# Optimization experiments

Hardware: AMD Instinct MI355X
Metric: run time of the kernel (lower is better)

Reference implementation:

```python
import jax, jax.numpy as jnp
import numpy as np

NUM_LAYERS, NUM_HEADS, DH, C = 5, 4, 32, 128
B, T, HH, WW = 2, 12, 32, 32


def conv2d(x, w, b):
    # x: (N, Cin, H, W), w: (Cout, Cin, 3, 3) same padding
    y = jax.lax.conv_general_dilated(x, w, window_strides=(1, 1), padding='SAME',
                                     dimension_numbers=('NCHW', 'OIHW', 'NCHW'))
    return y + b[None, :, None, None]


def sine_pos(length, depth):
    pos = jnp.arange(length, dtype=jnp.float32)[:, None]
    div = jnp.exp(jnp.arange(0, depth, 2, dtype=jnp.float32) * (-np.log(10000.0) / depth))
    pe = jnp.zeros((length, depth), dtype=jnp.float32)
    pe = pe.at[:, 0::2].set(jnp.sin(pos * div))
    pe = pe.at[:, 1::2].set(jnp.cos(pos * div))
    return pe[None, :, :, None, None]  # (1, L, dh, 1, 1) broadcasts over batch & spatial


def group_norm(x, scale, bias, groups=4, eps=1e-5):
    n, c, h, w = x.shape
    xg = x.reshape(n, groups, c // groups, h, w)
    mu = xg.mean(axis=(2, 3, 4), keepdims=True)
    var = ((xg - mu) ** 2).mean(axis=(2, 3, 4), keepdims=True)
    xg = (xg - mu) * jax.lax.rsqrt(var + eps)
    return xg.reshape(n, c, h, w) * scale[None, :, None, None] + bias[None, :, None, None]


def head_forward(x, pos, qw, qb, kvw, kvb, aw, ab):
    # x: (B, L, dh, H, W)
    b, l, c, h, w = x.shape
    xf = x.reshape(b * l, c, h, w)
    q = conv2d(xf, qw, qb).reshape(b, l, c, h, w) + pos
    v = conv2d(xf, kvw, kvb).reshape(b, l, c, h, w)  # k and v share features
    k = v + pos
    # pairwise concat: (B, Lq, Lk, 2*dh, H, W)
    qe = jnp.broadcast_to(q[:, :, None], (b, l, l, c, h, w))
    ke = jnp.broadcast_to(k[:, None, :], (b, l, l, c, h, w))
    qk = jnp.concatenate([qe, ke], axis=3).reshape(b * l * l, 2 * c, h, w)
    att = conv2d(qk, aw, ab).reshape(b, l, l, 1, h, w)
    att = jax.nn.softmax(att, axis=2)  # softmax over key-frame axis
    return jnp.sum(att * v[:, None], axis=2)  # (B, L, dh, H, W)


def reference(input_tensor, q_w, q_b, kv_w, kv_b, att_w, att_b,
              ff1_w, ff1_b, ff2_w, ff2_b, gn_w, gn_b):
    num_layers, num_heads = q_w.shape[0], q_w.shape[1]
    b, l, c, h, w = input_tensor.shape
    dh = c // num_heads
    pos = sine_pos(l, dh)
    out = input_tensor
    for li in range(num_layers):
        heads = [head_forward(out[:, :, i * dh:(i + 1) * dh], pos,
                              q_w[li, i], q_b[li, i], kv_w[li, i], kv_b[li, i],
                              att_w[li, i], att_b[li, i])
                 for i in range(num_heads)]
        att_out = jnp.concatenate(heads, axis=2) + out  # residual
        att_flat = att_out.reshape(b * l, c, h, w)
        ff = conv2d(jax.nn.relu(conv2d(att_flat, ff1_w[li], ff1_b[li])), ff2_w[li], ff2_b[li])
        y = group_norm(ff + att_flat, gn_w[li], gn_b[li])
        out = y.reshape(b, l, c, h, w)
    return out


def setup_inputs() -> dict:
    key = jax.random.key(0)
    ks = jax.random.split(key, 12)
    f = lambda k, s, sc=1.0: jax.random.normal(k, s, dtype=jnp.float32) * sc
    L, H = NUM_LAYERS, NUM_HEADS
    return {
        'input_tensor': f(ks[0], (B, T, C, HH, WW)),
        'q_w': f(ks[1], (L, H, DH, DH, 3, 3), 0.05),
        'q_b': f(ks[2], (L, H, DH), 0.05),
        'kv_w': f(ks[3], (L, H, DH, DH, 3, 3), 0.05),
        'kv_b': f(ks[4], (L, H, DH), 0.05),
        'att_w': f(ks[5], (L, H, 1, 2 * DH, 3, 3), 0.05),
        'att_b': f(ks[6], (L, H, 1), 0.05),
        'ff1_w': f(ks[7], (L, C, C, 3, 3), 0.03),
        'ff1_b': f(ks[8], (L, C), 0.03),
        'ff2_w': f(ks[9], (L, C, C, 3, 3), 0.03),
        'ff2_b': f(ks[10], (L, C), 0.03),
        'gn_w': jnp.ones((L, C), dtype=jnp.float32),
        'gn_b': jnp.zeros((L, C), dtype=jnp.float32),
    }
```

## Files before the change

kernel.cpp:

```cpp
#include <hip/hip_runtime.h>

#define NELEM 3145728
#define IMG 24
#define CH 128
#define HW 1024
#define PADP 1156
#define A2IMG 147968

using short8   = __attribute__((ext_vector_type(8))) short;
using ushort4v = __attribute__((ext_vector_type(4))) unsigned short;
using float4v  = __attribute__((ext_vector_type(4))) float;
using float16v = __attribute__((ext_vector_type(16))) float;

__device__ inline unsigned short f2bf(float f){
    union { float f; unsigned u; } c; c.f = f;
    return (unsigned short)((c.u + 0x7FFF + ((c.u >> 16) & 1)) >> 16);
}

__global__ __launch_bounds__(256) void k_prep(
    const float* __restrict__ ff1w, const float* __restrict__ ff2w,
    const float* __restrict__ kvw, const float* __restrict__ input,
    unsigned short* __restrict__ Wd, unsigned short* __restrict__ Wkv,
    unsigned short* __restrict__ A2v, float* __restrict__ cur)
{
    int gid = blockIdx.x * 256 + threadIdx.x;
    if (gid < 1474560) {
        int idx = gid;
        int li2 = idx / 147456, r1 = idx - li2 * 147456;
        int j = r1 & 7, co = (r1 >> 3) & 127;
        int kh = (r1 >> 10) & 1, k16 = (r1 >> 11) & 7, tap = r1 >> 14;
        int ci = k16 * 16 + kh * 8 + j;
        const float* base = ((li2 & 1) ? ff2w : ff1w) + (size_t)(li2 >> 1) * 147456;
        Wd[idx] = f2bf(base[(co * 128 + ci) * 9 + tap]);
    } else if (gid < 1658880) {
        int idx = gid - 1474560;
        int li = idx / 36864, r1 = idx - li * 36864;
        int j = r1 & 7, co = (r1 >> 3) & 127;
        int kh = (r1 >> 10) & 1, k16 = (r1 >> 11) & 1, tap = r1 >> 12;
        int h = co >> 5, colc = co & 31, cil = k16 * 16 + kh * 8 + j;
        Wkv[idx] = f2bf(kvw[((size_t)((li * 4 + h) * 32 + colc) * 32 + cil) * 9 + tap]);
    } else if (gid < 2064384) {
        int g2 = gid - 1658880;
        int c = g2 & 127, r = g2 >> 7;
        int bp = r % 132, img = r / 132;
        int pos;
        if (bp < 34) pos = bp;
        else if (bp < 68) pos = 33 * 34 + (bp - 34);
        else if (bp < 100) pos = (bp - 68 + 1) * 34;
        else pos = (bp - 100 + 1) * 34 + 33;
        A2v[(size_t)img * A2IMG + pos * 128 + c] = 0;
    } else {
        int g2 = gid - 2064384;
        int c4 = (g2 & 31) * 4, px = (g2 >> 5) & 1023, img = g2 >> 15;
        float4v v;
        #pragma unroll
        for (int j = 0; j < 4; j++)
            v[j] = input[((size_t)img * 128 + c4 + j) * HW + px];
        *(float4v*)(cur + ((size_t)img * HW + px) * 128 + c4) = v;
    }
}

__global__ __launch_bounds__(256, 2) void k_kvattn(
    const float* __restrict__ cur, const unsigned short* __restrict__ wkv,
    const float* __restrict__ kvb, const float* __restrict__ aw,
    const float* __restrict__ pstatp, const float* __restrict__ gw,
    const float* __restrict__ gb, float* __restrict__ v,
    float* __restrict__ ak, float* __restrict__ pstatz)
{
    const int img = blockIdx.x, h = blockIdx.y, y0 = blockIdx.z * 8;
    const int t = threadIdx.x;
    const int b = img / 12, l = img - b * 12;

    if (blockIdx.x == 0 && blockIdx.y == 0 && blockIdx.z == 0 && t < 192)
        pstatz[t] = 0.f;

    __shared__ float sxv[32 * 341];
    __shared__ unsigned short slab[408 * 40];
    __shared__ float spos[32], sbias[32], sgw[32], sgb[32];

    if (t < 32) {
        int j2 = t & ~1;
        float freq = __expf(-(float)j2 * 0.28782313662425576f);
        float ang = (float)l * freq;
        spos[t] = (t & 1) ? __cosf(ang) : __sinf(ang);
        sbias[t] = kvb[h * 32 + t];
        sgw[t] = gw ? gw[h * 32 + t] : 1.f;
        sgb[t] = gb ? gb[h * 32 + t] : 0.f;
    }
    float mu = 0.f, inv = 1.f;
    if (pstatp) {
        float S = pstatp[(img * 4 + h) * 2], Q = pstatp[(img * 4 + h) * 2 + 1];
        mu = S * (1.f / 32768.f);
        inv = rsqrtf(Q * (1.f / 32768.f) - mu * mu + 1e-5f);
    }
    __syncthreads();

    for (int u = t; u < 3264; u += 256) {
        int q = u & 7, p = u >> 3;
        int lr = p / 34, lc = p - lr * 34;
        int yr = y0 - 2 + lr, x = lc - 1;
        float4v val = (float4v){0.f, 0.f, 0.f, 0.f};
        if (yr >= 0 && yr < 32 && x >= 0 && x < 32) {
            val = *(const float4v*)(cur + ((size_t)img * HW + yr * 32 + x) * 128 + h * 32 + q * 4);
            #pragma unroll
            for (int j = 0; j < 4; j++)
                val[j] = (val[j] - mu) * inv * sgw[q * 4 + j] + sgb[q * 4 + j];
        }
        ushort4v o;
        #pragma unroll
        for (int j = 0; j < 4; j++) o[j] = f2bf(val[j]);
        *(ushort4v*)(slab + p * 40 + q * 4) = o;
    }
    __syncthreads();

    const int lane = t & 63, wave = t >> 6;
    const int colx = lane & 31, kh = lane >> 5;
    const short8* w8 = reinterpret_cast<const short8*>(wkv);

    for (int f = wave; f < 10; f += 4) {
        float16v acc;
        #pragma unroll
        for (int r = 0; r < 16; r++) acc[r] = 0.f;
        #pragma unroll
        for (int tap = 0; tap < 9; tap++) {
            const int ky = tap / 3, kx = tap - ky * 3;
            #pragma unroll
            for (int k16 = 0; k16 < 2; k16++) {
                short8 a = *reinterpret_cast<const short8*>(
                    slab + ((f + ky) * 34 + colx + kx) * 40 + k16 * 16 + kh * 8);
                short8 bf = w8[((tap * 2 + k16) * 2 + kh) * 128 + h * 32 + colx];
                acc = __builtin_amdgcn_mfma_f32_32x32x16_bf16(a, bf, acc, 0, 0, 0);
            }
        }
        const int yr = y0 - 1 + f;
        const bool rowin = (yr >= 0 && yr < 32);
        const bool vown = rowin && f >= 1 && f <= 8;
        const float posci = spos[colx], bb = sbias[colx];
        float* vrow = v + ((size_t)img * HW + yr * 32) * 128 + h * 32 + colx;
        #pragma unroll
        for (int r = 0; r < 16; r++) {
            int x2 = (r & 3) + 8 * (r >> 2) + 4 * kh;
            float val = rowin ? acc[r] + bb : 0.f;
            if (vown) vrow[(size_t)x2 * 128] = val;
            sxv[colx * 341 + f * 34 + x2 + 1] = rowin ? val + posci : 0.f;
        }
    }
    for (int u = t; u < 640; u += 256) {
        int ci = u & 31, r2 = u >> 5;
        sxv[ci * 341 + (r2 >> 1) * 34 + ((r2 & 1) ? 33 : 0)] = 0.f;
    }
    __syncthreads();

    const float* wb = aw + (h * 64 + 32) * 9;
    const int r = t >> 5, xx = t & 31;
    float acc2 = 0.f;
    #pragma unroll 4
    for (int ci = 0; ci < 32; ci++) {
        #pragma unroll
        for (int ky = 0; ky < 3; ky++)
            #pragma unroll
            for (int kx = 0; kx < 3; kx++)
                acc2 = fmaf(sxv[ci * 341 + (r + ky) * 34 + xx + kx],
                            wb[ci * 9 + ky * 3 + kx], acc2);
    }
    ak[((size_t)(b * 4 + h) * 12 + l) * HW + (y0 + r) * 32 + xx] = acc2;
}

template<bool SRC32, bool RELU, bool RES, bool EF32, bool EA2, bool STAT>
__global__ __launch_bounds__(256, 3) void k_conv(
    const unsigned short* __restrict__ a2in, const float* __restrict__ src32,
    const unsigned short* __restrict__ w2, const float* __restrict__ bias,
    const float* __restrict__ res, float* __restrict__ outf,
    unsigned short* __restrict__ outa2, float* __restrict__ pstat)
{
    const int y = blockIdx.x;
    const int img = blockIdx.y;
    const int t = threadIdx.x;
    const int wave = t >> 6, lane = t & 63;
    const int colx = lane & 31, kh = lane >> 5;
    const int cog = wave * 32;
    const int head = wave;

    __shared__ unsigned short sA[102 * 136];

    if (SRC32) {
        for (int u = t; u < 3264; u += 256) {
            int q = u & 31, p = u >> 5;
            int lr = p / 34, lc = p - lr * 34;
            int yr = y - 1 + lr, x = lc - 1;
            float4v val = (float4v){0.f, 0.f, 0.f, 0.f};
            if (yr >= 0 && yr < 32 && x >= 0 && x < 32)
                val = *(const float4v*)(src32 + ((size_t)img * HW + yr * 32 + x) * 128 + q * 4);
            ushort4v o;
            #pragma unroll
            for (int j = 0; j < 4; j++) o[j] = f2bf(val[j]);
            *(ushort4v*)(sA + p * 136 + q * 4) = o;
        }
    } else {
        const unsigned short* slab = a2in + (size_t)img * A2IMG + (size_t)y * 34 * 128;
        #pragma unroll
        for (int it = 0; it < 7; it++) {
            int u = it * 256 + t;
            if (u < 1632) {
                int px = u >> 4, g = u & 15;
                short8 vv = *reinterpret_cast<const short8*>(slab + px * 128 + g * 8);
                *reinterpret_cast<short8*>(sA + px * 136 + g * 8) = vv;
            }
        }
    }

    const short8* w8 = reinterpret_cast<const short8*>(w2);
    const int bl = kh * 128 + cog + colx;

    short8 bfr[2][8];
    auto loadB = [&](int tap, int buf){
        #pragma unroll
        for (int k16 = 0; k16 < 8; k16++)
            bfr[buf][k16] = w8[(tap * 8 + k16) * 256 + bl];
    };
    loadB(0, 0);

    float16v acc;
    #pragma unroll
    for (int r = 0; r < 16; r++) acc[r] = 0.f;

    __syncthreads();

    const int cibase = kh * 8;
    #pragma unroll
    for (int tap = 0; tap < 9; tap++) {
        if (tap + 1 < 9) loadB(tap + 1, (tap + 1) & 1);
        const int ky = tap / 3, kx = tap - ky * 3;
        const int pxl = ky * 34 + kx + colx;
        #pragma unroll
        for (int k16 = 0; k16 < 8; k16++) {
            short8 a = *reinterpret_cast<const short8*>(
                sA + pxl * 136 + cibase + k16 * 16);
            acc = __builtin_amdgcn_mfma_f32_32x32x16_bf16(
                a, bfr[tap & 1][k16], acc, 0, 0, 0);
        }
    }

    float s1 = 0.f, s2 = 0.f;
    const int co = cog + colx;
    const float bb = bias[co];
    #pragma unroll
    for (int r = 0; r < 16; r++) {
        int pxr = (r & 3) + 8 * (r >> 2) + 4 * kh;
        int px = y * 32 + pxr;
        float val = acc[r] + bb;
        if (RELU) val = fmaxf(val, 0.f);
        size_t ci = ((size_t)img * HW + px) * 128 + co;
        if (RES) val += res[ci];
        if (EF32) outf[ci] = val;
        if (EA2) {
            int pos = (y + 1) * 34 + pxr + 1;
            outa2[((size_t)img * PADP + pos) * 128 + co] = f2bf(val);
        }
        if (STAT) { s1 += val; s2 += val * val; }
    }
    if (STAT) {
        #pragma unroll
        for (int o = 32; o > 0; o >>= 1) {
            s1 += __shfl_down(s1, o); s2 += __shfl_down(s2, o);
        }
        if (lane == 0) {
            atomicAdd(&pstat[(img * 4 + head) * 2], s1);
            atomicAdd(&pstat[(img * 4 + head) * 2 + 1], s2);
        }
    }
}

__global__ __launch_bounds__(256) void k_wsum(const float* __restrict__ ak,
    const float* __restrict__ v, float* __restrict__ cur,
    const float* __restrict__ pstatp, const float* __restrict__ gw,
    const float* __restrict__ gb)
{
    int gid = blockIdx.x * 256 + threadIdx.x;
    int c4 = (gid & 31) * 4, px = (gid >> 5) & 1023, b = gid >> 15;
    int h = c4 >> 5;
    const float* wp = ak + ((b * 4 + h) * 12) * HW + px;
    float a[12], m = -1e30f;
    #pragma unroll
    for (int l = 0; l < 12; l++) { a[l] = wp[l * HW]; m = fmaxf(m, a[l]); }
    float ssum = 0.f;
    #pragma unroll
    for (int l = 0; l < 12; l++) { a[l] = __expf(a[l] - m); ssum += a[l]; }
    float invs = 1.f / ssum;
    float4v s = (float4v){0.f, 0.f, 0.f, 0.f};
    #pragma unroll
    for (int l = 0; l < 12; l++) {
        float4v vv = *(const float4v*)(v + (((size_t)(b * 12 + l) * HW) + px) * 128 + c4);
        #pragma unroll
        for (int j = 0; j < 4; j++) s[j] += a[l] * vv[j];
    }
    #pragma unroll
    for (int j = 0; j < 4; j++) s[j] *= invs;
    float gwv[4], gbv[4];
    #pragma unroll
    for (int j = 0; j < 4; j++) {
        gwv[j] = gw ? gw[c4 + j] : 1.f;
        gbv[j] = gb ? gb[c4 + j] : 0.f;
    }
    #pragma unroll
    for (int l = 0; l < 12; l++) {
        int img = b * 12 + l;
        float mu = 0.f, inv = 1.f;
        if (pstatp) {
            float S = pstatp[(img * 4 + h) * 2], Q = pstatp[(img * 4 + h) * 2 + 1];
            mu = S * (1.f / 32768.f);
            inv = rsqrtf(Q * (1.f / 32768.f) - mu * mu + 1e-5f);
        }
        size_t ci = (((size_t)img * HW) + px) * 128 + c4;
        float4v cv = *(float4v*)(cur + ci);
        #pragma unroll
        for (int j = 0; j < 4; j++)
            cv[j] = (cv[j] - mu) * inv * gwv[j] + gbv[j] + s[j];
        *(float4v*)(cur + ci) = cv;
    }
}

__global__ __launch_bounds__(256) void k_gnlast(const float* __restrict__ y,
    const float* __restrict__ pstat, const float* __restrict__ gw,
    const float* __restrict__ gb, float* __restrict__ outp)
{
    int gid = blockIdx.x * 256 + threadIdx.x;
    int px4 = (gid & 255) * 4, c = (gid >> 8) & 127, img = gid >> 15;
    int g = c >> 5;
    float S = pstat[(img * 4 + g) * 2], Q = pstat[(img * 4 + g) * 2 + 1];
    float mu = S * (1.f / 32768.f);
    float inv = rsqrtf(Q * (1.f / 32768.f) - mu * mu + 1e-5f);
    float gg = gw[c], bb = gb[c];
    float4v o;
    #pragma unroll
    for (int j = 0; j < 4; j++) {
        float val = y[((size_t)img * HW + px4 + j) * 128 + c];
        o[j] = (val - mu) * inv * gg + bb;
    }
    *(float4v*)(outp + ((size_t)img * 128 + c) * HW + px4) = o;
}

extern "C" void kernel_launch(void* const* d_in, const int* in_sizes, int n_in,
                              void* d_out, int out_size, void* d_ws, size_t ws_size,
                              hipStream_t stream)
{
    const float* input = (const float*)d_in[0];
    const float* kv_w  = (const float*)d_in[3];
    const float* kv_b  = (const float*)d_in[4];
    const float* att_w = (const float*)d_in[5];
    const float* ff1_w = (const float*)d_in[7];
    const float* ff1_b = (const float*)d_in[8];
    const float* ff2_w = (const float*)d_in[9];
    const float* ff2_b = (const float*)d_in[10];
    const float* gn_w  = (const float*)d_in[11];
    const float* gn_b  = (const float*)d_in[12];

    float* ws  = (float*)d_ws;
    float* cur = ws;
    float* ak  = ws + (size_t)NELEM;
    float* pstat = ak + 98304;
    unsigned short* W2d  = (unsigned short*)(pstat + 384);
    unsigned short* W2kv = W2d + 1474560;
    unsigned short* A2v  = W2kv + 184320;
    float* v    = (float*)d_out;
    float* outp = (float*)d_out;

    k_prep<<<11136, 256, 0, stream>>>(ff1_w, ff2_w, kv_w, input, W2d, W2kv, A2v, cur);

    for (int li = 0; li < 5; li++) {
        float* psC = pstat + (li & 1) * 192;
        const float* psP = li ? pstat + ((li - 1) & 1) * 192 : nullptr;
        const float* gwP = li ? gn_w + (li - 1) * 128 : nullptr;
        const float* gbP = li ? gn_b + (li - 1) * 128 : nullptr;

        k_kvattn<<<dim3(IMG, 4, 4), 256, 0, stream>>>(
            cur, W2kv + (size_t)li * 36864, kv_b + li * 128, att_w + (size_t)li * 2304,
            psP, gwP, gbP, v, ak, psC);
        k_wsum<<<256, 256, 0, stream>>>(ak, v, cur, psP, gwP, gbP);
        k_conv<true, true, false, false, true, false><<<dim3(32, IMG), 256, 0, stream>>>(
            nullptr, cur, W2d + (size_t)(li * 2 + 0) * 147456, ff1_b + li * 128,
            nullptr, nullptr, A2v, nullptr);
        k_conv<false, false, true, true, false, true><<<dim3(32, IMG), 256, 0, stream>>>(
            A2v, nullptr, W2d + (size_t)(li * 2 + 1) * 147456, ff2_b + li * 128,
            cur, cur, nullptr, psC);
    }
    k_gnlast<<<3072, 256, 0, stream>>>(cur, pstat + 0, gn_w + 4 * 128,
                                       gn_b + 4 * 128, outp);
}
```

Measured before the change: 507.4 us.

## Fuse FFN conv pair into one kernel with halo recompute, ping-pong activations

Replaces the two separate 3x3 conv launches of the feed-forward block with a single kernel. Each block computes the first conv for three rows (its own row plus halo rows), stores the ReLU output in shared memory as bf16, then runs the second conv. This removes the global bf16 intermediate buffer, its zero-padding setup and one launch per layer. The cost is recomputing first-conv rows (3x the MFMA work for conv1), more shared memory and fewer resident blocks. Activations now ping-pong between two buffers to avoid in-place hazards, and the input transpose in prep goes through a shared-memory tile so its global accesses are coalesced.

```diff
diff --git a/kernel.cpp b/kernel.cpp
--- a/kernel.cpp
+++ b/kernel.cpp
@@ -4,8 +4,6 @@
 #define IMG 24
 #define CH 128
 #define HW 1024
-#define PADP 1156
-#define A2IMG 147968
 
 using short8   = __attribute__((ext_vector_type(8))) short;
 using ushort4v = __attribute__((ext_vector_type(4))) unsigned short;
@@ -21,42 +19,42 @@
     const float* __restrict__ ff1w, const float* __restrict__ ff2w,
     const float* __restrict__ kvw, const float* __restrict__ input,
     unsigned short* __restrict__ Wd, unsigned short* __restrict__ Wkv,
-    unsigned short* __restrict__ A2v, float* __restrict__ cur)
-{
-    int gid = blockIdx.x * 256 + threadIdx.x;
-    if (gid < 1474560) {
-        int idx = gid;
+    float* __restrict__ cur)
+{
+    const int t = threadIdx.x;
+    __shared__ float tile[32 * 132];
+    if (blockIdx.x < 5760) {
+        int idx = blockIdx.x * 256 + t;
         int li2 = idx / 147456, r1 = idx - li2 * 147456;
         int j = r1 & 7, co = (r1 >> 3) & 127;
         int kh = (r1 >> 10) & 1, k16 = (r1 >> 11) & 7, tap = r1 >> 14;
         int ci = k16 * 16 + kh * 8 + j;
         const float* base = ((li2 & 1) ? ff2w : ff1w) + (size_t)(li2 >> 1) * 147456;
         Wd[idx] = f2bf(base[(co * 128 + ci) * 9 + tap]);
-    } else if (gid < 1658880) {
-        int idx = gid - 1474560;
+    } else if (blockIdx.x < 6480) {
+        int idx = (blockIdx.x - 5760) * 256 + t;
         int li = idx / 36864, r1 = idx - li * 36864;
         int j = r1 & 7, co = (r1 >> 3) & 127;
         int kh = (r1 >> 10) & 1, k16 = (r1 >> 11) & 1, tap = r1 >> 12;
         int h = co >> 5, colc = co & 31, cil = k16 * 16 + kh * 8 + j;
         Wkv[idx] = f2bf(kvw[((size_t)((li * 4 + h) * 32 + colc) * 32 + cil) * 9 + tap]);
-    } else if (gid < 2064384) {
-        int g2 = gid - 1658880;
-        int c = g2 & 127, r = g2 >> 7;
-        int bp = r % 132, img = r / 132;
-        int pos;
-        if (bp < 34) pos = bp;
-        else if (bp < 68) pos = 33 * 34 + (bp - 34);
-        else if (bp < 100) pos = (bp - 68 + 1) * 34;
-        else pos = (bp - 100 + 1) * 34 + 33;
-        A2v[(size_t)img * A2IMG + pos * 128 + c] = 0;
     } else {
-        int g2 = gid - 2064384;
-        int c4 = (g2 & 31) * 4, px = (g2 >> 5) & 1023, img = g2 >> 15;
-        float4v v;
-        #pragma unroll
-        for (int j = 0; j < 4; j++)
-            v[j] = input[((size_t)img * 128 + c4 + j) * HW + px];
-        *(float4v*)(cur + ((size_t)img * HW + px) * 128 + c4) = v;
+        int bb = blockIdx.x - 6480;
+        int img = bb >> 5, px0 = (bb & 31) * 32;
+        #pragma unroll
+        for (int it = 0; it < 4; it++) {
+            int c = it * 32 + (t >> 3), pxq = t & 7;
+            float4v val = *(const float4v*)(input + ((size_t)img * 128 + c) * HW + px0 + pxq * 4);
+            #pragma unroll
+            for (int j = 0; j < 4; j++) tile[(pxq * 4 + j) * 132 + c] = val[j];
+        }
+        __syncthreads();
+        #pragma unroll
+        for (int it = 0; it < 4; it++) {
+            int px = it * 8 + (t >> 5), cq = t & 31;
+            float4v o = *(float4v*)(tile + px * 132 + cq * 4);
+            *(float4v*)(cur + ((size_t)img * HW + px0 + px) * 128 + cq * 4) = o;
+        }
     }
 }
 
@@ -166,108 +164,129 @@
     ak[((size_t)(b * 4 + h) * 12 + l) * HW + (y0 + r) * 32 + xx] = acc2;
 }
 
-template<bool SRC32, bool RELU, bool RES, bool EF32, bool EA2, bool STAT>
-__global__ __launch_bounds__(256, 3) void k_conv(
-    const unsigned short* __restrict__ a2in, const float* __restrict__ src32,
-    const unsigned short* __restrict__ w2, const float* __restrict__ bias,
-    const float* __restrict__ res, float* __restrict__ outf,
-    unsigned short* __restrict__ outa2, float* __restrict__ pstat)
-{
-    const int y = blockIdx.x;
-    const int img = blockIdx.y;
+__global__ __launch_bounds__(256, 2) void k_ffn(
+    const float* __restrict__ cin, const unsigned short* __restrict__ w1,
+    const float* __restrict__ b1, const unsigned short* __restrict__ w2,
+    const float* __restrict__ b2, float* __restrict__ cout,
+    float* __restrict__ pstat)
+{
+    const int img = blockIdx.x, y = blockIdx.y;
     const int t = threadIdx.x;
     const int wave = t >> 6, lane = t & 63;
     const int colx = lane & 31, kh = lane >> 5;
     const int cog = wave * 32;
-    const int head = wave;
-
-    __shared__ unsigned short sA[102 * 136];
-
-    if (SRC32) {
-        for (int u = t; u < 3264; u += 256) {
-            int q = u & 31, p = u >> 5;
-            int lr = p / 34, lc = p - lr * 34;
-            int yr = y - 1 + lr, x = lc - 1;
-            float4v val = (float4v){0.f, 0.f, 0.f, 0.f};
-            if (yr >= 0 && yr < 32 && x >= 0 && x < 32)
-                val = *(const float4v*)(src32 + ((size_t)img * HW + yr * 32 + x) * 128 + q * 4);
-            ushort4v o;
-            #pragma unroll
-            for (int j = 0; j < 4; j++) o[j] = f2bf(val[j]);
-            *(ushort4v*)(sA + p * 136 + q * 4) = o;
-        }
-    } else {
-        const unsigned short* slab = a2in + (size_t)img * A2IMG + (size_t)y * 34 * 128;
-        #pragma unroll
-        for (int it = 0; it < 7; it++) {
-            int u = it * 256 + t;
-            if (u < 1632) {
-                int px = u >> 4, g = u & 15;
-                short8 vv = *reinterpret_cast<const short8*>(slab + px * 128 + g * 8);
-                *reinterpret_cast<short8*>(sA + px * 136 + g * 8) = vv;
+
+    __shared__ unsigned short s1[170 * 136];
+    __shared__ unsigned short s2[102 * 136];
+
+    for (int u = t; u < 5440; u += 256) {
+        int q = u & 31, p = u >> 5;
+        int lr = p / 34, lc = p - lr * 34;
+        int yr = y - 2 + lr, x = lc - 1;
+        float4v val = (float4v){0.f, 0.f, 0.f, 0.f};
+        if (yr >= 0 && yr < 32 && x >= 0 && x < 32)
+            val = *(const float4v*)(cin + ((size_t)img * HW + yr * 32 + x) * 128 + q * 4);
+        ushort4v o;
+        #pragma unroll
+        for (int j = 0; j < 4; j++) o[j] = f2bf(val[j]);
+        *(ushort4v*)(s1 + p * 136 + q * 4) = o;
+    }
+
+    const short8* w8a = reinterpret_cast<const short8*>(w1);
+    const short8* w8b = reinterpret_cast<const short8*>(w2);
+    const int bl = kh * 128 + cog + colx;
+
+    short8 bfr[2][8];
+    auto loadB1 = [&](int tap, int buf){
+        #pragma unroll
+        for (int k16 = 0; k16 < 8; k16++)
+            bfr[buf][k16] = w8a[(tap * 8 + k16) * 256 + bl];
+    };
+    auto loadB2 = [&](int tap, int buf){
+        #pragma unroll
+        for (int k16 = 0; k16 < 8; k16++)
+            bfr[buf][k16] = w8b[(tap * 8 + k16) * 256 + bl];
+    };
+    loadB1(0, 0);
+
+    float16v acc[3];
+    #pragma unroll
+    for (int f = 0; f < 3; f++)
+        #pragma unroll
+        for (int r = 0; r < 16; r++) acc[f][r] = 0.f;
+
+    __syncthreads();
+
+    #pragma unroll
+    for (int tap = 0; tap < 9; tap++) {
+        if (tap + 1 < 9) loadB1(tap + 1, (tap + 1) & 1);
+        const int ky = tap / 3, kx = tap - ky * 3;
+        #pragma unroll
+        for (int k16 = 0; k16 < 8; k16++) {
+            short8 bv = bfr[tap & 1][k16];
+            #pragma unroll
+            for (int f = 0; f < 3; f++) {
+                short8 a = *reinterpret_cast<const short8*>(
+                    s1 + ((f + ky) * 34 + kx + colx) * 136 + kh * 8 + k16 * 16);
+                acc[f] = __builtin_amdgcn_mfma_f32_32x32x16_bf16(a, bv, acc[f], 0, 0, 0);
             }
         }
     }
 
-    const short8* w8 = reinterpret_cast<const short8*>(w2);
-    const int bl = kh * 128 + cog + colx;
-
-    short8 bfr[2][8];
-    auto loadB = [&](int tap, int buf){
-        #pragma unroll
-        for (int k16 = 0; k16 < 8; k16++)
-            bfr[buf][k16] = w8[(tap * 8 + k16) * 256 + bl];
-    };
-    loadB(0, 0);
-
-    float16v acc;
-    #pragma unroll
-    for (int r = 0; r < 16; r++) acc[r] = 0.f;
-
+    {
+        const int co = cog + colx;
+        const float bb1 = b1[co];
+        #pragma unroll
+        for (int f = 0; f < 3; f++) {
+            const bool rowin = (y - 1 + f >= 0) && (y - 1 + f < 32);
+            #pragma unroll
+            for (int r = 0; r < 16; r++) {
+                int x2 = (r & 3) + 8 * (r >> 2) + 4 * kh;
+                float val = rowin ? fmaxf(acc[f][r] + bb1, 0.f) : 0.f;
+                s2[(f * 34 + x2 + 1) * 136 + co] = f2bf(val);
+            }
+        }
+    }
+    for (int u = t; u < 768; u += 256) {
+        int c = u & 127, rr = u >> 7;
+        s2[((rr >> 1) * 34 + ((rr & 1) ? 33 : 0)) * 136 + c] = 0;
+    }
+    loadB2(0, 0);
     __syncthreads();
 
-    const int cibase = kh * 8;
+    float16v a2;
+    #pragma unroll
+    for (int r = 0; r < 16; r++) a2[r] = 0.f;
     #pragma unroll
     for (int tap = 0; tap < 9; tap++) {
-        if (tap + 1 < 9) loadB(tap + 1, (tap + 1) & 1);
+        if (tap + 1 < 9) loadB2(tap + 1, (tap + 1) & 1);
         const int ky = tap / 3, kx = tap - ky * 3;
-        const int pxl = ky * 34 + kx + colx;
         #pragma unroll
         for (int k16 = 0; k16 < 8; k16++) {
             short8 a = *reinterpret_cast<const short8*>(
-                sA + pxl * 136 + cibase + k16 * 16);
-            acc = __builtin_amdgcn_mfma_f32_32x32x16_bf16(
-                a, bfr[tap & 1][k16], acc, 0, 0, 0);
-        }
-    }
-
-    float s1 = 0.f, s2 = 0.f;
+                s2 + (ky * 34 + kx + colx) * 136 + kh * 8 + k16 * 16);
+            a2 = __builtin_amdgcn_mfma_f32_32x32x16_bf16(a, bfr[tap & 1][k16], a2, 0, 0, 0);
+        }
+    }
+
+    float s1s = 0.f, s2s = 0.f;
     const int co = cog + colx;
-    const float bb = bias[co];
+    const float bb2 = b2[co];
     #pragma unroll
     for (int r = 0; r < 16; r++) {
-        int pxr = (r & 3) + 8 * (r >> 2) + 4 * kh;
-        int px = y * 32 + pxr;
-        float val = acc[r] + bb;
-        if (RELU) val = fmaxf(val, 0.f);
-        size_t ci = ((size_t)img * HW + px) * 128 + co;
-        if (RES) val += res[ci];
-        if (EF32) outf[ci] = val;
-        if (EA2) {
-            int pos = (y + 1) * 34 + pxr + 1;
-            outa2[((size_t)img * PADP + pos) * 128 + co] = f2bf(val);
-        }
-        if (STAT) { s1 += val; s2 += val * val; }
-    }
-    if (STAT) {
-        #pragma unroll
-        for (int o = 32; o > 0; o >>= 1) {
-            s1 += __shfl_down(s1, o); s2 += __shfl_down(s2, o);
-        }
-        if (lane == 0) {
-            atomicAdd(&pstat[(img * 4 + head) * 2], s1);
-            atomicAdd(&pstat[(img * 4 + head) * 2 + 1], s2);
-        }
+        int x2 = (r & 3) + 8 * (r >> 2) + 4 * kh;
+        size_t ci = ((size_t)img * HW + y * 32 + x2) * 128 + co;
+        float val = a2[r] + bb2 + cin[ci];
+        cout[ci] = val;
+        s1s += val; s2s += val * val;
+    }
+    #pragma unroll
+    for (int o = 32; o > 0; o >>= 1) {
+        s1s += __shfl_down(s1s, o); s2s += __shfl_down(s2s, o);
+    }
+    if (lane == 0) {
+        atomicAdd(&pstat[(img * 4 + wave) * 2], s1s);
+        atomicAdd(&pstat[(img * 4 + wave) * 2 + 1], s2s);
     }
 }
 
@@ -356,34 +375,33 @@
     const float* gn_b  = (const float*)d_in[12];
 
     float* ws  = (float*)d_ws;
-    float* cur = ws;
-    float* ak  = ws + (size_t)NELEM;
+    float* c0  = ws;
+    float* c1  = c0 + (size_t)NELEM;
+    float* ak  = c1 + (size_t)NELEM;
     float* pstat = ak + 98304;
     unsigned short* W2d  = (unsigned short*)(pstat + 384);
     unsigned short* W2kv = W2d + 1474560;
-    unsigned short* A2v  = W2kv + 184320;
     float* v    = (float*)d_out;
     float* outp = (float*)d_out;
 
-    k_prep<<<11136, 256, 0, stream>>>(ff1_w, ff2_w, kv_w, input, W2d, W2kv, A2v, cur);
+    k_prep<<<7248, 256, 0, stream>>>(ff1_w, ff2_w, kv_w, input, W2d, W2kv, c0);
 
     for (int li = 0; li < 5; li++) {
+        float* cin  = (li & 1) ? c1 : c0;
+        float* cout = (li & 1) ? c0 : c1;
         float* psC = pstat + (li & 1) * 192;
         const float* psP = li ? pstat + ((li - 1) & 1) * 192 : nullptr;
         const float* gwP = li ? gn_w + (li - 1) * 128 : nullptr;
         const float* gbP = li ? gn_b + (li - 1) * 128 : nullptr;
 
         k_kvattn<<<dim3(IMG, 4, 4), 256, 0, stream>>>(
-            cur, W2kv + (size_t)li * 36864, kv_b + li * 128, att_w + (size_t)li * 2304,
+            cin, W2kv + (size_t)li * 36864, kv_b + li * 128, att_w + (size_t)li * 2304,
             psP, gwP, gbP, v, ak, psC);
-        k_wsum<<<256, 256, 0, stream>>>(ak, v, cur, psP, gwP, gbP);
-        k_conv<true, true, false, false, true, false><<<dim3(32, IMG), 256, 0, stream>>>(
-            nullptr, cur, W2d + (size_t)(li * 2 + 0) * 147456, ff1_b + li * 128,
-            nullptr, nullptr, A2v, nullptr);
-        k_conv<false, false, true, true, false, true><<<dim3(32, IMG), 256, 0, stream>>>(
-            A2v, nullptr, W2d + (size_t)(li * 2 + 1) * 147456, ff2_b + li * 128,
-            cur, cur, nullptr, psC);
-    }
-    k_gnlast<<<3072, 256, 0, stream>>>(cur, pstat + 0, gn_w + 4 * 128,
+        k_wsum<<<256, 256, 0, stream>>>(ak, v, cin, psP, gwP, gbP);
+        k_ffn<<<dim3(IMG, 32), 256, 0, stream>>>(
+            cin, W2d + (size_t)(li * 2 + 0) * 147456, ff1_b + li * 128,
+            W2d + (size_t)(li * 2 + 1) * 147456, ff2_b + li * 128, cout, psC);
+    }
+    k_gnlast<<<3072, 256, 0, stream>>>(c1, pstat + 0, gn_w + 4 * 128,
                                        gn_b + 4 * 128, outp);
 }
```

Result: slower. 538.8 us (+6.2%).
